# Kernel tuning notes

Hardware: AMD Instinct MI355X
Metric: run time of the kernel (lower is better)

## Reference

```python
import jax, jax.numpy as jnp
import numpy as np

N = 100_000      # nodes
E = 1_600_000    # edges
F_IN = 128       # n_features == conv_dim1..3
F_OUT = 256      # concat_dim
G = 2000         # number of graphs in the batch
EPS = 1e-5       # BatchNorm eps


def _xavier(k, shape):
    fan_in, fan_out = shape[-2], shape[-1]
    lim = float(np.sqrt(6.0 / (fan_in + fan_out)))
    return jax.random.uniform(k, shape, jnp.float32, -lim, lim)


def setup_inputs() -> dict:
    key = jax.random.key(0)
    ks = jax.random.split(key, 8)
    x = jax.random.normal(ks[0], (N, F_IN), jnp.float32)
    edge_index = jax.random.randint(ks[1], (2, E), 0, N, dtype=jnp.int64)
    batch = jnp.sort(jax.random.randint(ks[2], (N,), 0, G, dtype=jnp.int64))
    # layers 1..5: F_IN -> F_IN (stacked), layer 6: F_IN -> F_OUT
    Wi = _xavier(ks[3], (5, F_IN, F_IN))   # ARMA init_weight per layer
    Wr = _xavier(ks[4], (5, F_IN, F_IN))   # ARMA root_weight per layer
    b = jnp.zeros((5, F_IN), jnp.float32)  # ARMA bias per layer
    g = jnp.ones((5, F_IN), jnp.float32)   # BN gamma
    be = jnp.zeros((5, F_IN), jnp.float32) # BN beta
    Wi6 = _xavier(ks[5], (F_IN, F_OUT))
    Wr6 = _xavier(ks[6], (F_IN, F_OUT))
    b6 = jnp.zeros((F_OUT,), jnp.float32)
    g6 = jnp.ones((F_OUT,), jnp.float32)
    be6 = jnp.zeros((F_OUT,), jnp.float32)
    return dict(x=x, edge_index=edge_index, batch=batch, Wi=Wi, Wr=Wr, b=b,
                g=g, be=be, Wi6=Wi6, Wr6=Wr6, b6=b6, g6=g6, be6=be6)


def _arma(x, norm, row, col, Wi_l, Wr_l, b_l):
    # ARMAConv (num_stacks=1, num_layers=1, act=ReLU):
    #   out = ReLU( A_norm @ (x W_init) + x W_root + b )
    h = x @ Wi_l                                           # [N, F_out]
    msg = h[row] * norm[:, None]                           # gather + scale, [E, F_out]
    agg = jax.ops.segment_sum(msg, col, num_segments=N)    # scatter-add
    return jax.nn.relu(agg + x @ Wr_l + b_l)


def _bn(x, gamma, beta):
    # BatchNorm1d, training mode (biased batch variance)
    mu = x.mean(axis=0)
    var = x.var(axis=0)
    return gamma * (x - mu) * jax.lax.rsqrt(var + EPS) + beta


def reference(x, edge_index, batch, Wi, Wr, b, g, be, Wi6, Wr6, b6, g6, be6):
    row, col = edge_index[0], edge_index[1]
    # gcn_norm without self loops: D^-1/2 A D^-1/2 edge weights
    deg = jax.ops.segment_sum(jnp.ones((E,), x.dtype), col, num_segments=N)
    dinv = jnp.where(deg > 0, jax.lax.rsqrt(deg), 0.0)
    norm = dinv[row] * dinv[col]                           # [E]

    h = x
    for l in range(5):  # fixed small layer count
        h = _arma(h, norm, row, col, Wi[l], Wr[l], b[l])   # outer F.relu is idempotent
        h = _bn(h, g[l], be[l])
    h = _arma(h, norm, row, col, Wi6, Wr6, b6)
    h = _bn(h, g6, be6)
    # global_add_pool over graph ids; dropout = identity (deterministic baseline)
    out = jax.ops.segment_sum(h, batch, num_segments=G)    # [G, F_OUT]
    return out
```

## Files before the change

kernel.cpp:

```cpp
#include <hip/hip_runtime.h>

#define Nn 100000
#define NP 100001
#define Ee 1600000
#define Gg 2000
#define EPSf 1e-5f

typedef unsigned short ushort_t;
typedef __attribute__((ext_vector_type(8))) short short8;
typedef __attribute__((ext_vector_type(4))) float f32x4;
typedef __attribute__((ext_vector_type(4))) unsigned u32x4;

__device__ inline float bf2f(unsigned int u) {
    union { unsigned int i; float f; } v; v.i = u << 16; return v.f;
}
__device__ inline unsigned short f2bf(float f) {
    unsigned int x = __float_as_uint(f);
    unsigned int r = (x + 0x7fffu + ((x >> 16) & 1u)) >> 16;
    return (unsigned short)r;
}
__device__ inline int ldidx(const void* a, int i, int i64) {
    return i64 ? (int)((const long long*)a)[i] : ((const int*)a)[i];
}
__device__ inline float ldflt(const void* p, long long i, int f32) {
    return f32 ? ((const float*)p)[i] : bf2f(((const ushort_t*)p)[i]);
}


__global__ void k_flags(const void* gones, const void* ei, int* flags) {
    if (threadIdx.x == 0 && blockIdx.x == 0) {
        unsigned w = *(const unsigned*)gones;
        flags[0] = (w == 0x3F800000u) ? 1 : 0;
        const int* e = (const int*)ei;
        int nz = 0;
        for (int i = 0; i < 256; i++) nz |= e[2 * i + 1];
        flags[1] = nz ? 0 : 1;
    }
}


__global__ void k_hist(const void* __restrict__ ei, int* __restrict__ deg, const int* __restrict__ flags) {
    int i = blockIdx.x * 256 + threadIdx.x;
    if (i < Ee) {
        int c = ldidx(ei, Ee + i, flags[1]);
        atomicAdd(&deg[c], 1);
    }
}

__global__ void k_dinv(const int* __restrict__ deg, float* __restrict__ dinv) {
    int i = blockIdx.x * 256 + threadIdx.x;
    if (i < Nn) { int d = deg[i]; dinv[i] = d > 0 ? rsqrtf((float)d) : 0.f; }
}

__global__ void k_scan1(const int* __restrict__ deg, int* __restrict__ off, int* __restrict__ part) {
    __shared__ int sh[1024];
    int i = blockIdx.x * 1024 + threadIdx.x;
    int v = (i < Nn) ? ((deg[i] + 3) & ~3) : 0;
    sh[threadIdx.x] = v;
    __syncthreads();
    for (int ofs = 1; ofs < 1024; ofs <<= 1) {
        int t = 0;
        if ((int)threadIdx.x >= ofs) t = sh[threadIdx.x - ofs];
        __syncthreads();
        sh[threadIdx.x] += t;
        __syncthreads();
    }
    if (i < Nn) off[i] = sh[threadIdx.x] - v;
    if (threadIdx.x == 1023) part[blockIdx.x] = sh[1023];
}

__global__ void k_scan2(int* part, int nb) {
    if (threadIdx.x == 0 && blockIdx.x == 0) {
        int run = 0;
        for (int i = 0; i < nb; i++) { int t = part[i]; part[i] = run; run += t; }
        part[nb] = run;
    }
}

__global__ void k_scan3(int* __restrict__ off, const int* __restrict__ part, int* __restrict__ cursor) {
    int i = blockIdx.x * 256 + threadIdx.x;
    if (i < Nn) {
        int v = off[i] + part[i >> 10];
        off[i] = v;
        cursor[i] = v;
    }
    if (i == 0) off[Nn] = part[98];
}

__global__ void k_fillp(const void* __restrict__ ei, int* __restrict__ cursor,
                        int* __restrict__ srcS, const int* __restrict__ flags) {
    int range = blockIdx.x & 7;
    int e = (blockIdx.x >> 3) * 256 + threadIdx.x;
    if (e < Ee) {
        int i64 = flags[1];
        int c = ldidx(ei, Ee + e, i64);
        if (c >= range * 12500 && c < (range + 1) * 12500) {
            int r = ldidx(ei, e, i64);
            int p = atomicAdd(&cursor[c], 1);
            srcS[p] = r;
        }
    }
}

__global__ void k_pad(const int* __restrict__ cursor, const int* __restrict__ off,
                      int* __restrict__ srcS) {
    int i = blockIdx.x * 256 + threadIdx.x;
    if (i < Nn) {
        int e = off[i + 1];
        for (int p = cursor[i]; p < e; p++) srcS[p] = Nn;
    }
}

__global__ void k_zrow(ushort_t* __restrict__ Hi) {
    int t = threadIdx.x;
    int fc = t >> 4, j = t & 15;
    Hi[((size_t)fc * NP + Nn) * 16 + j] = 0;
}

__global__ void k_cvtp(const void* b, const void* b6, const void* g, const void* g6,
                       const void* be, const void* be6,
                       float* __restrict__ biasF, float* __restrict__ gF,
                       float* __restrict__ beF, const int* __restrict__ flags) {
    int i = blockIdx.x * 256 + threadIdx.x;
    if (i >= 2688) return;
    int grp = i / 896, r = i - grp * 896;
    int f32 = flags[0];
    const void* srcs[6] = { b, b6, g, g6, be, be6 };
    float* dsts[3] = { biasF, gF, beF };
    const void* s = (r < 640) ? srcs[grp * 2] : srcs[grp * 2 + 1];
    int idx = (r < 640) ? r : r - 640;
    dsts[grp][r] = ldflt(s, idx, f32);
}

__global__ void k_cvtx(const void* __restrict__ x, ushort_t* __restrict__ xq, const int* __restrict__ flags) {
    int node = blockIdx.x * 256 + threadIdx.x;
    int fc = blockIdx.y;
    if (node < Nn) {
        union { ushort_t u[16]; u32x4 v[2]; } t;
        if (flags[0]) {
            const float* p = (const float*)x + (size_t)node * 128 + fc * 16;
#pragma unroll
            for (int j = 0; j < 16; j++) t.u[j] = f2bf(p[j]);
        } else {
            const ushort_t* p = (const ushort_t*)x + (size_t)node * 128 + fc * 16;
#pragma unroll
            for (int j = 0; j < 16; j++) t.u[j] = p[j];
        }
        u32x4* d = (u32x4*)(xq + ((size_t)fc * Nn + node) * 16);
        d[0] = t.v[0]; d[1] = t.v[1];
    }
}

__global__ void k_pack(const void* __restrict__ Wi, const void* __restrict__ Wr,
                       const void* __restrict__ Wi6, const void* __restrict__ Wr6,
                       ushort_t* __restrict__ Bp, const int* __restrict__ flags) {
    int idx = blockIdx.x * 256 + threadIdx.x;
    if (idx >= 229376) return;
    int f32 = flags[0];
    if (idx < 163840) {
        int l = idx / 32768, rem = idx - l * 32768;
        int kg = rem / 2048, rem2 = rem - kg * 2048;
        int n = rem2 / 8, j = rem2 - n * 8;
        int k = kg * 8 + j;
        float v = (n < 128) ? ldflt(Wi, (l * 128 + k) * 128 + n, f32)
                            : ldflt(Wr, (l * 128 + k) * 128 + (n - 128), f32);
        Bp[idx] = f2bf(v);
    } else {
        int idx2 = idx - 163840;
        int kg = idx2 / 4096, rem2 = idx2 - kg * 4096;
        int n = rem2 / 8, j = rem2 - n * 8;
        int k = kg * 8 + j;
        float v = (n < 256) ? ldflt(Wi6, k * 256 + n, f32) : ldflt(Wr6, k * 256 + (n - 256), f32);
        Bp[idx] = f2bf(v);
    }
}

__global__ void k_fold(const ushort_t* __restrict__ Bp, const float* __restrict__ stat,
                       const float* __restrict__ gamma, const float* __restrict__ beta,
                       const float* __restrict__ bias,
                       ushort_t* __restrict__ Bp2, float* __restrict__ hcorr, int ncat) {
    __shared__ float red[128];
    int n = blockIdx.x, k = threadIdx.x;
    int fhalf = ncat >> 1;
    float mu = stat[k] * (1.f / Nn);
    float var = stat[128 + k] * (1.f / Nn) - mu * mu;
    float rs = rsqrtf(var + EPSf);
    float s = gamma[k] * rs;
    float h = beta[k] - s * mu;
    size_t idx = ((size_t)(k >> 3) * ncat + n) * 8 + (k & 7);
    float w = bf2f(Bp[idx]);
    Bp2[idx] = f2bf(w * s);
    red[k] = h * w;
    __syncthreads();
    for (int m = 64; m > 0; m >>= 1) { if (k < m) red[k] += red[k + m]; __syncthreads(); }
    if (k == 0) hcorr[n] = red[0] + (n >= fhalf ? bias[n - fhalf] : 0.f);
}

__global__ void k_h0(const float* __restrict__ bias, float* __restrict__ hc, int ncat) {
    int n = blockIdx.x * 256 + threadIdx.x;
    if (n < ncat) hc[n] = n >= (ncat >> 1) ? bias[n - (ncat >> 1)] : 0.f;
}


__global__ __launch_bounds__(256) void k_gemm(
        const ushort_t* __restrict__ Aq,
        const ushort_t* __restrict__ Bp, const float* __restrict__ hcorr,
        const float* __restrict__ dinv,
        ushort_t* __restrict__ Hi, ushort_t* __restrict__ yq, int ncat) {
    __shared__ ushort_t stage[32 * 264];
    const int tid = threadIdx.x, lane = tid & 63, wid = tid >> 6;
    const int q = lane >> 4, l15 = lane & 15;
    const int fhalf = ncat >> 1;
    const int colW = blockIdx.y * 256 + wid * 64;
    const int row0 = blockIdx.x * 64;

    short8 bfr[4][4];
    float hc[4];
#pragma unroll
    for (int kk = 0; kk < 4; kk++) {
        int kg = kk * 4 + q;
#pragma unroll
        for (int ct = 0; ct < 4; ct++)
            bfr[kk][ct] = *(const short8*)(Bp + ((size_t)kg * ncat + colW + ct * 16 + l15) * 8);
    }
#pragma unroll
    for (int ct = 0; ct < 4; ct++) hc[ct] = hcorr[colW + ct * 16 + l15];

    f32x4 acc[4][4];
    f32x4 z; z.x = 0.f; z.y = 0.f; z.z = 0.f; z.w = 0.f;
#pragma unroll
    for (int rt = 0; rt < 4; rt++)
#pragma unroll
        for (int ct = 0; ct < 4; ct++) acc[rt][ct] = z;

#pragma unroll
    for (int kk = 0; kk < 4; kk++) {
        int kg = kk * 4 + q;
        const ushort_t* ap = Aq + (size_t)(kg >> 1) * Nn * 16 + (kg & 1) * 8;
        short8 af[4];
#pragma unroll
        for (int rt = 0; rt < 4; rt++) {
            int node = row0 + rt * 16 + l15;
            if (node >= Nn) node = Nn - 1;
            af[rt] = *(const short8*)(ap + (size_t)node * 16);
        }
#pragma unroll
        for (int rt = 0; rt < 4; rt++)
#pragma unroll
            for (int ct = 0; ct < 4; ct++)
                acc[rt][ct] = __builtin_amdgcn_mfma_f32_16x16x32_bf16(af[rt], bfr[kk][ct], acc[rt][ct], 0, 0, 0);
    }

#pragma unroll
    for (int half = 0; half < 2; half++) {
        __syncthreads();
#pragma unroll
        for (int ct = 0; ct < 4; ct++) {
            int lcol = wid * 64 + ct * 16 + l15;
            bool isHi = (blockIdx.y * 256 + lcol) < fhalf;
#pragma unroll
            for (int rt2 = 0; rt2 < 2; rt2++) {
                int rt = half * 2 + rt2;
#pragma unroll
                for (int r = 0; r < 4; r++) {
                    int grow = row0 + rt * 16 + q * 4 + r;
                    int gr = grow < Nn ? grow : 0;
                    float v = acc[rt][ct][r] + hc[ct];
                    if (isHi) v *= dinv[gr];
                    stage[(rt2 * 16 + q * 4 + r) * 264 + lcol] = f2bf(v);
                }
            }
        }
        __syncthreads();
        for (int chunk = tid; chunk < 512; chunk += 256) {
            int cg = chunk & 15, rl = chunk >> 4;
            int node = row0 + half * 32 + rl;
            if (node < Nn) {
                int gc0 = blockIdx.y * 256 + cg * 16;
                const u32x4* sp = (const u32x4*)&stage[rl * 264 + cg * 16];
                u32x4 v0 = sp[0], v1 = sp[1];
                ushort_t* dst = (gc0 < fhalf)
                    ? Hi + ((size_t)(gc0 >> 4) * NP + node) * 16
                    : yq + ((size_t)((gc0 - fhalf) >> 4) * Nn + node) * 16;
                u32x4* dp = (u32x4*)dst;
                dp[0] = v0; dp[1] = v1;
            }
        }
    }
}


__global__ __launch_bounds__(256) void k_agg8(const int* __restrict__ off, const int* __restrict__ src,
                                              const float* __restrict__ dinv, const unsigned* __restrict__ Hi2,
                                              unsigned* __restrict__ yq, float* __restrict__ stat,
                                              int F, int fcbase) {
    const int tid = threadIdx.x;
    const int w = tid >> 6, lane = tid & 63;
    const int sub = lane >> 3, fl = lane & 7;
    const int e2 = (fl >> 1) & 3;
    const int h  = fl & 1;
    const int fc = fcbase + (blockIdx.x & 7);
    const int T = blockIdx.x >> 3;
    const char* __restrict__ gbase = (const char*)Hi2 + (size_t)fc * ((size_t)NP * 32) + h * 16;

    float stS[8], stQ[8];
#pragma unroll
    for (int j = 0; j < 8; j++) { stS[j] = 0.f; stQ[j] = 0.f; }

#pragma unroll
    for (int pass = 0; pass < 4; pass++) {
        int node = T * 128 + pass * 32 + w * 8 + sub;
        bool valid = node < Nn;
        int p0 = 0, p1 = 0;
        if (valid) { p0 = off[node]; p1 = off[node + 1]; }
        float a[8];
#pragma unroll
        for (int j = 0; j < 8; j++) a[j] = 0.f;
        int p = p0;
        for (; p + 15 < p1; p += 16) {
            int s0 = src[p + e2];
            int s1 = src[p + 4 + e2];
            int s2 = src[p + 8 + e2];
            int s3 = src[p + 12 + e2];
            u32x4 g0 = *(const u32x4*)(gbase + (size_t)((unsigned)s0 << 5));
            u32x4 g1 = *(const u32x4*)(gbase + (size_t)((unsigned)s1 << 5));
            u32x4 g2 = *(const u32x4*)(gbase + (size_t)((unsigned)s2 << 5));
            u32x4 g3 = *(const u32x4*)(gbase + (size_t)((unsigned)s3 << 5));
#pragma unroll
            for (int d = 0; d < 4; d++) {
                a[2*d]   += bf2f(g0[d] & 0xffffu); a[2*d+1] += bf2f(g0[d] >> 16);
                a[2*d]   += bf2f(g1[d] & 0xffffu); a[2*d+1] += bf2f(g1[d] >> 16);
                a[2*d]   += bf2f(g2[d] & 0xffffu); a[2*d+1] += bf2f(g2[d] >> 16);
                a[2*d]   += bf2f(g3[d] & 0xffffu); a[2*d+1] += bf2f(g3[d] >> 16);
            }
        }
        if (p + 7 < p1) {
            int s0 = src[p + e2];
            int s1 = src[p + 4 + e2];
            u32x4 g0 = *(const u32x4*)(gbase + (size_t)((unsigned)s0 << 5));
            u32x4 g1 = *(const u32x4*)(gbase + (size_t)((unsigned)s1 << 5));
#pragma unroll
            for (int d = 0; d < 4; d++) {
                a[2*d]   += bf2f(g0[d] & 0xffffu); a[2*d+1] += bf2f(g0[d] >> 16);
                a[2*d]   += bf2f(g1[d] & 0xffffu); a[2*d+1] += bf2f(g1[d] >> 16);
            }
            p += 8;
        }
        if (p < p1) {
            int s0 = src[p + e2];
            u32x4 g0 = *(const u32x4*)(gbase + (size_t)((unsigned)s0 << 5));
#pragma unroll
            for (int d = 0; d < 4; d++) {
                a[2*d]   += bf2f(g0[d] & 0xffffu); a[2*d+1] += bf2f(g0[d] >> 16);
            }
        }
#pragma unroll
        for (int j = 0; j < 8; j++) {
            a[j] += __shfl_xor(a[j], 2, 64);
            a[j] += __shfl_xor(a[j], 4, 64);
        }
        if (valid && fl < 2) {
            float dv = dinv[node];
            u32x4* yp = (u32x4*)(yq + ((size_t)fc * Nn + node) * 8 + h * 4);
            u32x4 uv = *yp;
#pragma unroll
            for (int d = 0; d < 4; d++) {
                float vlo = fmaxf(bf2f(uv[d] & 0xffffu) + dv * a[2*d],   0.f);
                float vhi = fmaxf(bf2f(uv[d] >> 16)     + dv * a[2*d+1], 0.f);
                uv[d] = (unsigned)f2bf(vlo) | ((unsigned)f2bf(vhi) << 16);
                stS[2*d]   += vlo; stQ[2*d]   += vlo * vlo;
                stS[2*d+1] += vhi; stQ[2*d+1] += vhi * vhi;
            }
            *yp = uv;
        }
    }
#pragma unroll
    for (int j = 0; j < 8; j++) {
        stS[j] += __shfl_xor(stS[j], 8, 64);
        stQ[j] += __shfl_xor(stQ[j], 8, 64);
        stS[j] += __shfl_xor(stS[j], 16, 64);
        stQ[j] += __shfl_xor(stQ[j], 16, 64);
        stS[j] += __shfl_xor(stS[j], 32, 64);
        stQ[j] += __shfl_xor(stQ[j], 32, 64);
    }
    __shared__ float red[4][2][8][2];
    if (lane < 2) {
#pragma unroll
        for (int j = 0; j < 8; j++) {
            red[w][lane][j][0] = stS[j];
            red[w][lane][j][1] = stQ[j];
        }
    }
    __syncthreads();
    if (tid < 32) {
        int hh = tid >> 4, r = tid & 15, j = r >> 1, m = r & 1;
        float s = red[0][hh][j][m] + red[1][hh][j][m] + red[2][hh][j][m] + red[3][hh][j][m];
        int f = fc * 16 + hh * 8 + j;
        atomicAdd(&stat[m * F + f], s);
    }
}


__device__ inline int lb(const void* a, int n, int key, int i64) {
    int lo = 0, hi = n;
    while (lo < hi) { int mid = (lo + hi) >> 1; if (ldidx(a, mid, i64) < key) lo = mid + 1; else hi = mid; }
    return lo;
}

__global__ void k_pool(const ushort_t* __restrict__ y6q, const float* __restrict__ stat,
                       const float* __restrict__ g6, const float* __restrict__ be6,
                       const void* __restrict__ batch, void* __restrict__ out,
                       const int* __restrict__ flags) {
    int g = blockIdx.x;
    int f = threadIdx.x;
    int i64 = flags[1];
    int start = lb(batch, Nn, g, i64);
    int end = lb(batch, Nn, g + 1, i64);
    const ushort_t* yp = y6q + (size_t)(f >> 4) * Nn * 16 + (f & 15);
    float s = 0.f;
    for (int n = start; n < end; n++) s += bf2f(yp[(size_t)n * 16]);
    int cnt = end - start;
    float mu = stat[f] * (1.f / Nn);
    float var = stat[256 + f] * (1.f / Nn) - mu * mu;
    float rs = rsqrtf(var + EPSf);
    float val = g6[f] * rs * (s - (float)cnt * mu) + (float)cnt * be6[f];
    if (flags[0]) ((float*)out)[(size_t)g * 256 + f] = val;
    else          ((ushort_t*)out)[(size_t)g * 256 + f] = f2bf(val);
}


extern "C" void kernel_launch(void* const* d_in, const int* in_sizes, int n_in,
                              void* d_out, int out_size, void* d_ws, size_t ws_size,
                              hipStream_t stream) {
    const void* x    = d_in[0];
    const void* ei   = d_in[1];
    const void* batch= d_in[2];
    const void* Wi   = d_in[3];
    const void* Wr   = d_in[4];
    const void* b    = d_in[5];
    const void* g    = d_in[6];
    const void* be   = d_in[7];
    const void* Wi6  = d_in[8];
    const void* Wr6  = d_in[9];
    const void* b6   = d_in[10];
    const void* g6   = d_in[11];
    const void* be6  = d_in[12];

    char* p = (char*)d_ws;
    auto alloc = [&](size_t bytes) { char* r = p; p += (bytes + 511) & ~(size_t)511; return r; };
    ushort_t* HiB  = (ushort_t*)alloc((size_t)NP * 256 * 2);
    ushort_t* xq   = (ushort_t*)alloc((size_t)Nn * 128 * 2);
    ushort_t* yAq  = (ushort_t*)alloc((size_t)Nn * 128 * 2);
    ushort_t* yBq  = (ushort_t*)alloc((size_t)Nn * 128 * 2);
    ushort_t* y6q  = (ushort_t*)alloc((size_t)Nn * 256 * 2);
    int* srcS      = (int*)alloc(((size_t)Ee + 4 * Nn + 64) * 4);
    int* off       = (int*)alloc((size_t)(Nn + 1) * 4);
    int* cursor    = (int*)alloc((size_t)Nn * 4);
    int* deg       = (int*)alloc((size_t)Nn * 4);
    float* dinv    = (float*)alloc((size_t)Nn * 4);
    int* part      = (int*)alloc(128 * 4);
    float* statsA  = (float*)alloc(6 * 512 * 4);
    ushort_t* Bp   = (ushort_t*)alloc(229376 * 2);
    ushort_t* Bp2  = (ushort_t*)alloc(65536 * 2);
    float* hcorrA  = (float*)alloc(512 * 4);
    int* flags     = (int*)alloc(2 * 4);
    float* biasF   = (float*)alloc(896 * 4);
    float* gF      = (float*)alloc(896 * 4);
    float* beF     = (float*)alloc(896 * 4);
    const unsigned* Hi2 = (const unsigned*)HiB;

    const int AGG_GRID = 782 * 8;
    const int GEMM_GRID = 1563;

    k_flags<<<1, 64, 0, stream>>>(g, ei, flags);
    k_cvtp<<<11, 256, 0, stream>>>(b, b6, g, g6, be, be6, biasF, gF, beF, flags);

    hipMemsetAsync(deg, 0, (size_t)Nn * 4, stream);
    hipMemsetAsync(statsA, 0, 6 * 512 * 4, stream);
    k_hist<<<6250, 256, 0, stream>>>(ei, deg, flags);
    k_dinv<<<391, 256, 0, stream>>>(deg, dinv);
    k_scan1<<<98, 1024, 0, stream>>>(deg, off, part);
    k_scan2<<<1, 64, 0, stream>>>(part, 98);
    k_scan3<<<391, 256, 0, stream>>>(off, part, cursor);
    k_fillp<<<50000, 256, 0, stream>>>(ei, cursor, srcS, flags);
    k_pad<<<391, 256, 0, stream>>>(cursor, off, srcS);
    k_zrow<<<1, 256, 0, stream>>>(HiB);
    k_pack<<<896, 256, 0, stream>>>(Wi, Wr, Wi6, Wr6, Bp, flags);
    k_cvtx<<<dim3(391, 8), 256, 0, stream>>>(x, xq, flags);
    k_h0<<<1, 256, 0, stream>>>(biasF, hcorrA, 256);

    k_gemm<<<dim3(GEMM_GRID, 1), 256, 0, stream>>>(xq, Bp, hcorrA, dinv, HiB, yAq, 256);
    k_agg8<<<AGG_GRID, 256, 0, stream>>>(off, srcS, dinv, Hi2, (unsigned*)yAq, statsA, 128, 0);
    k_fold<<<256, 128, 0, stream>>>(Bp + 32768, statsA, gF, beF, biasF + 128, Bp2, hcorrA, 256);

    k_gemm<<<dim3(GEMM_GRID, 1), 256, 0, stream>>>(yAq, Bp2, hcorrA, dinv, HiB, yBq, 256);
    k_agg8<<<AGG_GRID, 256, 0, stream>>>(off, srcS, dinv, Hi2, (unsigned*)yBq, statsA + 512, 128, 0);
    k_fold<<<256, 128, 0, stream>>>(Bp + 65536, statsA + 512, gF + 128, beF + 128, biasF + 256, Bp2, hcorrA, 256);

    k_gemm<<<dim3(GEMM_GRID, 1), 256, 0, stream>>>(yBq, Bp2, hcorrA, dinv, HiB, yAq, 256);
    k_agg8<<<AGG_GRID, 256, 0, stream>>>(off, srcS, dinv, Hi2, (unsigned*)yAq, statsA + 1024, 128, 0);
    k_fold<<<256, 128, 0, stream>>>(Bp + 98304, statsA + 1024, gF + 256, beF + 256, biasF + 384, Bp2, hcorrA, 256);

    k_gemm<<<dim3(GEMM_GRID, 1), 256, 0, stream>>>(yAq, Bp2, hcorrA, dinv, HiB, yBq, 256);
    k_agg8<<<AGG_GRID, 256, 0, stream>>>(off, srcS, dinv, Hi2, (unsigned*)yBq, statsA + 1536, 128, 0);
    k_fold<<<256, 128, 0, stream>>>(Bp + 131072, statsA + 1536, gF + 384, beF + 384, biasF + 512, Bp2, hcorrA, 256);

    k_gemm<<<dim3(GEMM_GRID, 1), 256, 0, stream>>>(yBq, Bp2, hcorrA, dinv, HiB, yAq, 256);
    k_agg8<<<AGG_GRID, 256, 0, stream>>>(off, srcS, dinv, Hi2, (unsigned*)yAq, statsA + 2048, 128, 0);
    k_fold<<<512, 128, 0, stream>>>(Bp + 163840, statsA + 2048, gF + 512, beF + 512, biasF + 640, Bp2, hcorrA, 512);

    k_gemm<<<dim3(GEMM_GRID, 2), 256, 0, stream>>>(yAq, Bp2, hcorrA, dinv, HiB, y6q, 512);
    k_agg8<<<AGG_GRID, 256, 0, stream>>>(off, srcS, dinv, Hi2, (unsigned*)y6q, statsA + 2560, 256, 0);
    k_agg8<<<AGG_GRID, 256, 0, stream>>>(off, srcS, dinv, Hi2, (unsigned*)y6q, statsA + 2560, 256, 8);
    k_pool<<<Gg, 256, 0, stream>>>(y6q, statsA + 2560, gF + 640, be6 ? beF + 640 : beF + 640, batch, d_out, flags);
}
```

Before: 1.145 ms.

## Split CSR aggregation by source-node half and widen feature planes to 32

Edges are partitioned into two CSRs by source index (below or above 50000), and aggregation runs in two passes. The first pass writes fp32 partial sums into scratch buffers, and the second adds the other half and applies the ReLU epilogue and BN statistics. Each pass gathers from only half the node rows, which is meant to keep the gathered working set resident in cache. Feature planes are also widened from 16 to 32 bf16 (64-byte rows) across the GEMM, conversion and pooling code. In exchange it adds extra launches, a second scan/fill pipeline, and fp32 partial-sum write and read traffic, and it reuses activation buffers as scratch.

```diff
diff --git a/kernel.cpp b/kernel.cpp
--- a/kernel.cpp
+++ b/kernel.cpp
@@ -5,6 +5,7 @@
 #define Ee 1600000
 #define Gg 2000
 #define EPSf 1e-5f
+#define NHALF 50000
 
 typedef unsigned short ushort_t;
 typedef __attribute__((ext_vector_type(8))) short short8;
@@ -39,17 +40,21 @@
 }
 
 
-__global__ void k_hist(const void* __restrict__ ei, int* __restrict__ deg, const int* __restrict__ flags) {
+__global__ void k_hist(const void* __restrict__ ei, int* __restrict__ degA, int* __restrict__ degB,
+                       const int* __restrict__ flags) {
     int i = blockIdx.x * 256 + threadIdx.x;
     if (i < Ee) {
-        int c = ldidx(ei, Ee + i, flags[1]);
-        atomicAdd(&deg[c], 1);
-    }
-}
-
-__global__ void k_dinv(const int* __restrict__ deg, float* __restrict__ dinv) {
+        int i64 = flags[1];
+        int c = ldidx(ei, Ee + i, i64);
+        int r = ldidx(ei, i, i64);
+        atomicAdd((r < NHALF) ? &degA[c] : &degB[c], 1);
+    }
+}
+
+__global__ void k_dinv(const int* __restrict__ degA, const int* __restrict__ degB,
+                       float* __restrict__ dinv) {
     int i = blockIdx.x * 256 + threadIdx.x;
-    if (i < Nn) { int d = deg[i]; dinv[i] = d > 0 ? rsqrtf((float)d) : 0.f; }
+    if (i < Nn) { int d = degA[i] + degB[i]; dinv[i] = d > 0 ? rsqrtf((float)d) : 0.f; }
 }
 
 __global__ void k_scan1(const int* __restrict__ deg, int* __restrict__ off, int* __restrict__ part) {
@@ -87,8 +92,8 @@
     if (i == 0) off[Nn] = part[98];
 }
 
-__global__ void k_fillp(const void* __restrict__ ei, int* __restrict__ cursor,
-                        int* __restrict__ srcS, const int* __restrict__ flags) {
+__global__ void k_fillp(const void* __restrict__ ei, int* __restrict__ curA, int* __restrict__ curB,
+                        int* __restrict__ srcA, int* __restrict__ srcB, const int* __restrict__ flags) {
     int range = blockIdx.x & 7;
     int e = (blockIdx.x >> 3) * 256 + threadIdx.x;
     if (e < Ee) {
@@ -96,25 +101,29 @@
         int c = ldidx(ei, Ee + e, i64);
         if (c >= range * 12500 && c < (range + 1) * 12500) {
             int r = ldidx(ei, e, i64);
-            int p = atomicAdd(&cursor[c], 1);
-            srcS[p] = r;
-        }
-    }
-}
-
-__global__ void k_pad(const int* __restrict__ cursor, const int* __restrict__ off,
-                      int* __restrict__ srcS) {
+            if (r < NHALF) { int p = atomicAdd(&curA[c], 1); srcA[p] = r; }
+            else           { int p = atomicAdd(&curB[c], 1); srcB[p] = r; }
+        }
+    }
+}
+
+__global__ void k_pad(const int* __restrict__ curA, const int* __restrict__ offA, int* __restrict__ srcA,
+                      const int* __restrict__ curB, const int* __restrict__ offB, int* __restrict__ srcB) {
     int i = blockIdx.x * 256 + threadIdx.x;
     if (i < Nn) {
-        int e = off[i + 1];
-        for (int p = cursor[i]; p < e; p++) srcS[p] = Nn;
-    }
-}
-
-__global__ void k_zrow(ushort_t* __restrict__ Hi) {
+        int e = offA[i + 1];
+        for (int p = curA[i]; p < e; p++) srcA[p] = Nn;
+        e = offB[i + 1];
+        for (int p = curB[i]; p < e; p++) srcB[p] = Nn;
+    }
+}
+
+__global__ void k_zrow(unsigned* __restrict__ Hi) {
     int t = threadIdx.x;
-    int fc = t >> 4, j = t & 15;
-    Hi[((size_t)fc * NP + Nn) * 16 + j] = 0;
+    if (t < 128) {
+        int pl = t >> 4, j = t & 15;
+        Hi[((size_t)pl * NP + Nn) * 16 + j] = 0;
+    }
 }
 
 __global__ void k_cvtp(const void* b, const void* b6, const void* g, const void* g6,
@@ -146,7 +155,7 @@
 #pragma unroll
             for (int j = 0; j < 16; j++) t.u[j] = p[j];
         }
-        u32x4* d = (u32x4*)(xq + ((size_t)fc * Nn + node) * 16);
+        u32x4* d = (u32x4*)(xq + ((size_t)(fc >> 1) * Nn + node) * 32 + (fc & 1) * 16);
         d[0] = t.v[0]; d[1] = t.v[1];
     }
 }
@@ -236,13 +245,13 @@
 #pragma unroll
     for (int kk = 0; kk < 4; kk++) {
         int kg = kk * 4 + q;
-        const ushort_t* ap = Aq + (size_t)(kg >> 1) * Nn * 16 + (kg & 1) * 8;
+        const ushort_t* ap = Aq + (size_t)(kg >> 2) * ((size_t)Nn * 32) + (kg & 3) * 8;
         short8 af[4];
 #pragma unroll
         for (int rt = 0; rt < 4; rt++) {
             int node = row0 + rt * 16 + l15;
             if (node >= Nn) node = Nn - 1;
-            af[rt] = *(const short8*)(ap + (size_t)node * 16);
+            af[rt] = *(const short8*)(ap + (size_t)node * 32);
         }
 #pragma unroll
         for (int rt = 0; rt < 4; rt++)
@@ -279,9 +288,13 @@
                 int gc0 = blockIdx.y * 256 + cg * 16;
                 const u32x4* sp = (const u32x4*)&stage[rl * 264 + cg * 16];
                 u32x4 v0 = sp[0], v1 = sp[1];
-                ushort_t* dst = (gc0 < fhalf)
-                    ? Hi + ((size_t)(gc0 >> 4) * NP + node) * 16
-                    : yq + ((size_t)((gc0 - fhalf) >> 4) * Nn + node) * 16;
+                ushort_t* dst;
+                if (gc0 < fhalf) {
+                    dst = Hi + ((size_t)(gc0 >> 5) * NP + node) * 32 + (gc0 & 16);
+                } else {
+                    int gy = gc0 - fhalf;
+                    dst = yq + ((size_t)(gy >> 5) * Nn + node) * 32 + (gy & 16);
+                }
                 u32x4* dp = (u32x4*)dst;
                 dp[0] = v0; dp[1] = v1;
             }
@@ -290,22 +303,79 @@
 }
 
 
-__global__ __launch_bounds__(256) void k_agg8(const int* __restrict__ off, const int* __restrict__ src,
-                                              const float* __restrict__ dinv, const unsigned* __restrict__ Hi2,
-                                              unsigned* __restrict__ yq, float* __restrict__ stat,
-                                              int F, int fcbase) {
+__device__ __forceinline__ void edge_sum(const int* __restrict__ src, int p0, int p1,
+                                         const char* __restrict__ gbase, int e2,
+                                         float* __restrict__ a) {
+    int p = p0;
+    for (; p + 15 < p1; p += 16) {
+        int b0 = p + 2 * e2;
+        int sa0 = src[b0],      sa1 = src[b0 + 1];
+        int sb0 = src[b0 + 4],  sb1 = src[b0 + 5];
+        int sc0 = src[b0 + 8],  sc1 = src[b0 + 9];
+        int sd0 = src[b0 + 12], sd1 = src[b0 + 13];
+        u32x4 g0 = *(const u32x4*)(gbase + ((size_t)(unsigned)sa0 << 6));
+        u32x4 g1 = *(const u32x4*)(gbase + ((size_t)(unsigned)sa1 << 6));
+        u32x4 g2 = *(const u32x4*)(gbase + ((size_t)(unsigned)sb0 << 6));
+        u32x4 g3 = *(const u32x4*)(gbase + ((size_t)(unsigned)sb1 << 6));
+        u32x4 g4 = *(const u32x4*)(gbase + ((size_t)(unsigned)sc0 << 6));
+        u32x4 g5 = *(const u32x4*)(gbase + ((size_t)(unsigned)sc1 << 6));
+        u32x4 g6 = *(const u32x4*)(gbase + ((size_t)(unsigned)sd0 << 6));
+        u32x4 g7 = *(const u32x4*)(gbase + ((size_t)(unsigned)sd1 << 6));
+#pragma unroll
+        for (int d = 0; d < 4; d++) {
+            a[2*d] += bf2f(g0[d] & 0xffffu); a[2*d+1] += bf2f(g0[d] >> 16);
+            a[2*d] += bf2f(g1[d] & 0xffffu); a[2*d+1] += bf2f(g1[d] >> 16);
+            a[2*d] += bf2f(g2[d] & 0xffffu); a[2*d+1] += bf2f(g2[d] >> 16);
+            a[2*d] += bf2f(g3[d] & 0xffffu); a[2*d+1] += bf2f(g3[d] >> 16);
+            a[2*d] += bf2f(g4[d] & 0xffffu); a[2*d+1] += bf2f(g4[d] >> 16);
+            a[2*d] += bf2f(g5[d] & 0xffffu); a[2*d+1] += bf2f(g5[d] >> 16);
+            a[2*d] += bf2f(g6[d] & 0xffffu); a[2*d+1] += bf2f(g6[d] >> 16);
+            a[2*d] += bf2f(g7[d] & 0xffffu); a[2*d+1] += bf2f(g7[d] >> 16);
+        }
+    }
+    if (p + 7 < p1) {
+        int b0 = p + 2 * e2;
+        int sa0 = src[b0],     sa1 = src[b0 + 1];
+        int sb0 = src[b0 + 4], sb1 = src[b0 + 5];
+        u32x4 g0 = *(const u32x4*)(gbase + ((size_t)(unsigned)sa0 << 6));
+        u32x4 g1 = *(const u32x4*)(gbase + ((size_t)(unsigned)sa1 << 6));
+        u32x4 g2 = *(const u32x4*)(gbase + ((size_t)(unsigned)sb0 << 6));
+        u32x4 g3 = *(const u32x4*)(gbase + ((size_t)(unsigned)sb1 << 6));
+#pragma unroll
+        for (int d = 0; d < 4; d++) {
+            a[2*d] += bf2f(g0[d] & 0xffffu); a[2*d+1] += bf2f(g0[d] >> 16);
+            a[2*d] += bf2f(g1[d] & 0xffffu); a[2*d+1] += bf2f(g1[d] >> 16);
+            a[2*d] += bf2f(g2[d] & 0xffffu); a[2*d+1] += bf2f(g2[d] >> 16);
+            a[2*d] += bf2f(g3[d] & 0xffffu); a[2*d+1] += bf2f(g3[d] >> 16);
+        }
+        p += 8;
+    }
+    if (p < p1) {
+        int b0 = p + 2 * e2;
+        int sa0 = src[b0], sa1 = src[b0 + 1];
+        u32x4 g0 = *(const u32x4*)(gbase + ((size_t)(unsigned)sa0 << 6));
+        u32x4 g1 = *(const u32x4*)(gbase + ((size_t)(unsigned)sa1 << 6));
+#pragma unroll
+        for (int d = 0; d < 4; d++) {
+            a[2*d] += bf2f(g0[d] & 0xffffu); a[2*d+1] += bf2f(g0[d] >> 16);
+            a[2*d] += bf2f(g1[d] & 0xffffu); a[2*d+1] += bf2f(g1[d] >> 16);
+        }
+    }
+}
+
+__global__ __launch_bounds__(256) void k_aggA(const int* __restrict__ off, const int* __restrict__ src,
+                                              const unsigned* __restrict__ Hi2,
+                                              float* __restrict__ pAlo, float* __restrict__ pAhi,
+                                              int fcpbase) {
     const int tid = threadIdx.x;
     const int w = tid >> 6, lane = tid & 63;
     const int sub = lane >> 3, fl = lane & 7;
-    const int e2 = (fl >> 1) & 3;
-    const int h  = fl & 1;
-    const int fc = fcbase + (blockIdx.x & 7);
-    const int T = blockIdx.x >> 3;
-    const char* __restrict__ gbase = (const char*)Hi2 + (size_t)fc * ((size_t)NP * 32) + h * 16;
-
-    float stS[8], stQ[8];
-#pragma unroll
-    for (int j = 0; j < 8; j++) { stS[j] = 0.f; stQ[j] = 0.f; }
+    const int e2 = fl >> 2, qd = fl & 3;
+    const int combo = blockIdx.x & 7;
+    const int fcl = combo & 3;
+    const int T = (blockIdx.x >> 3) + 391 * (combo >> 2);
+    const char* __restrict__ gbase = (const char*)Hi2 + (size_t)(fcpbase + fcl) * ((size_t)NP * 64) + qd * 16;
+    float* __restrict__ pbase = ((fcl & 2) ? pAhi : pAlo) + (size_t)(fcl & 1) * ((size_t)Nn * 32) + qd * 8;
 
 #pragma unroll
     for (int pass = 0; pass < 4; pass++) {
@@ -316,62 +386,69 @@
         float a[8];
 #pragma unroll
         for (int j = 0; j < 8; j++) a[j] = 0.f;
-        int p = p0;
-        for (; p + 15 < p1; p += 16) {
-            int s0 = src[p + e2];
-            int s1 = src[p + 4 + e2];
-            int s2 = src[p + 8 + e2];
-            int s3 = src[p + 12 + e2];
-            u32x4 g0 = *(const u32x4*)(gbase + (size_t)((unsigned)s0 << 5));
-            u32x4 g1 = *(const u32x4*)(gbase + (size_t)((unsigned)s1 << 5));
-            u32x4 g2 = *(const u32x4*)(gbase + (size_t)((unsigned)s2 << 5));
-            u32x4 g3 = *(const u32x4*)(gbase + (size_t)((unsigned)s3 << 5));
+        edge_sum(src, p0, p1, gbase, e2, a);
+#pragma unroll
+        for (int j = 0; j < 8; j++) a[j] += __shfl_xor(a[j], 4, 64);
+        if (valid && e2 == 0) {
+            float* pr = pbase + (size_t)node * 32;
+            f32x4 v0, v1;
+            v0.x = a[0]; v0.y = a[1]; v0.z = a[2]; v0.w = a[3];
+            v1.x = a[4]; v1.y = a[5]; v1.z = a[6]; v1.w = a[7];
+            *(f32x4*)pr = v0;
+            *(f32x4*)(pr + 4) = v1;
+        }
+    }
+}
+
+__global__ __launch_bounds__(256) void k_aggB(const int* __restrict__ off, const int* __restrict__ src,
+                                              const float* __restrict__ dinv, const unsigned* __restrict__ Hi2,
+                                              const float* __restrict__ pAlo, const float* __restrict__ pAhi,
+                                              unsigned* __restrict__ yq, float* __restrict__ stat,
+                                              int F, int fcpbase) {
+    const int tid = threadIdx.x;
+    const int w = tid >> 6, lane = tid & 63;
+    const int sub = lane >> 3, fl = lane & 7;
+    const int e2 = fl >> 2, qd = fl & 3;
+    const int combo = blockIdx.x & 7;
+    const int fcl = combo & 3;
+    const int fcp = fcpbase + fcl;
+    const int T = (blockIdx.x >> 3) + 391 * (combo >> 2);
+    const char* __restrict__ gbase = (const char*)Hi2 + (size_t)fcp * ((size_t)NP * 64) + qd * 16;
+    const float* __restrict__ pbase = ((fcl & 2) ? pAhi : pAlo) + (size_t)(fcl & 1) * ((size_t)Nn * 32) + qd * 8;
+
+    float stS[8], stQ[8];
+#pragma unroll
+    for (int j = 0; j < 8; j++) { stS[j] = 0.f; stQ[j] = 0.f; }
+
+#pragma unroll
+    for (int pass = 0; pass < 4; pass++) {
+        int node = T * 128 + pass * 32 + w * 8 + sub;
+        bool valid = node < Nn;
+        int p0 = 0, p1 = 0;
+        if (valid) { p0 = off[node]; p1 = off[node + 1]; }
+        float a[8];
+#pragma unroll
+        for (int j = 0; j < 8; j++) a[j] = 0.f;
+        edge_sum(src, p0, p1, gbase, e2, a);
+#pragma unroll
+        for (int j = 0; j < 8; j++) a[j] += __shfl_xor(a[j], 4, 64);
+        if (valid && e2 == 0) {
+            float dv = dinv[node];
+            const float* pr = pbase + (size_t)node * 32;
+            f32x4 pa0 = *(const f32x4*)pr;
+            f32x4 pa1 = *(const f32x4*)(pr + 4);
+            float pav[8] = { pa0.x, pa0.y, pa0.z, pa0.w, pa1.x, pa1.y, pa1.z, pa1.w };
+            unsigned* yp = yq + ((size_t)fcp * Nn + node) * 16 + qd * 4;
+            u32x4 uv = *(u32x4*)yp;
 #pragma unroll
             for (int d = 0; d < 4; d++) {
-                a[2*d]   += bf2f(g0[d] & 0xffffu); a[2*d+1] += bf2f(g0[d] >> 16);
-                a[2*d]   += bf2f(g1[d] & 0xffffu); a[2*d+1] += bf2f(g1[d] >> 16);
-                a[2*d]   += bf2f(g2[d] & 0xffffu); a[2*d+1] += bf2f(g2[d] >> 16);
-                a[2*d]   += bf2f(g3[d] & 0xffffu); a[2*d+1] += bf2f(g3[d] >> 16);
-            }
-        }
-        if (p + 7 < p1) {
-            int s0 = src[p + e2];
-            int s1 = src[p + 4 + e2];
-            u32x4 g0 = *(const u32x4*)(gbase + (size_t)((unsigned)s0 << 5));
-            u32x4 g1 = *(const u32x4*)(gbase + (size_t)((unsigned)s1 << 5));
-#pragma unroll
-            for (int d = 0; d < 4; d++) {
-                a[2*d]   += bf2f(g0[d] & 0xffffu); a[2*d+1] += bf2f(g0[d] >> 16);
-                a[2*d]   += bf2f(g1[d] & 0xffffu); a[2*d+1] += bf2f(g1[d] >> 16);
-            }
-            p += 8;
-        }
-        if (p < p1) {
-            int s0 = src[p + e2];
-            u32x4 g0 = *(const u32x4*)(gbase + (size_t)((unsigned)s0 << 5));
-#pragma unroll
-            for (int d = 0; d < 4; d++) {
-                a[2*d]   += bf2f(g0[d] & 0xffffu); a[2*d+1] += bf2f(g0[d] >> 16);
-            }
-        }
-#pragma unroll
-        for (int j = 0; j < 8; j++) {
-            a[j] += __shfl_xor(a[j], 2, 64);
-            a[j] += __shfl_xor(a[j], 4, 64);
-        }
-        if (valid && fl < 2) {
-            float dv = dinv[node];
-            u32x4* yp = (u32x4*)(yq + ((size_t)fc * Nn + node) * 8 + h * 4);
-            u32x4 uv = *yp;
-#pragma unroll
-            for (int d = 0; d < 4; d++) {
-                float vlo = fmaxf(bf2f(uv[d] & 0xffffu) + dv * a[2*d],   0.f);
-                float vhi = fmaxf(bf2f(uv[d] >> 16)     + dv * a[2*d+1], 0.f);
+                float vlo = fmaxf(bf2f(uv[d] & 0xffffu) + dv * (pav[2*d]   + a[2*d]),   0.f);
+                float vhi = fmaxf(bf2f(uv[d] >> 16)     + dv * (pav[2*d+1] + a[2*d+1]), 0.f);
                 uv[d] = (unsigned)f2bf(vlo) | ((unsigned)f2bf(vhi) << 16);
                 stS[2*d]   += vlo; stQ[2*d]   += vlo * vlo;
                 stS[2*d+1] += vhi; stQ[2*d+1] += vhi * vhi;
             }
-            *yp = uv;
+            *(u32x4*)yp = uv;
         }
     }
 #pragma unroll
@@ -383,8 +460,8 @@
         stS[j] += __shfl_xor(stS[j], 32, 64);
         stQ[j] += __shfl_xor(stQ[j], 32, 64);
     }
-    __shared__ float red[4][2][8][2];
-    if (lane < 2) {
+    __shared__ float red[4][4][8][2];
+    if (lane < 4) {
 #pragma unroll
         for (int j = 0; j < 8; j++) {
             red[w][lane][j][0] = stS[j];
@@ -392,11 +469,10 @@
         }
     }
     __syncthreads();
-    if (tid < 32) {
-        int hh = tid >> 4, r = tid & 15, j = r >> 1, m = r & 1;
-        float s = red[0][hh][j][m] + red[1][hh][j][m] + red[2][hh][j][m] + red[3][hh][j][m];
-        int f = fc * 16 + hh * 8 + j;
-        atomicAdd(&stat[m * F + f], s);
+    if (tid < 64) {
+        int qdx = tid >> 4, j = (tid >> 1) & 7, m = tid & 1;
+        float s = red[0][qdx][j][m] + red[1][qdx][j][m] + red[2][qdx][j][m] + red[3][qdx][j][m];
+        atomicAdd(&stat[m * F + fcp * 32 + qdx * 8 + j], s);
     }
 }
 
@@ -416,9 +492,9 @@
     int i64 = flags[1];
     int start = lb(batch, Nn, g, i64);
     int end = lb(batch, Nn, g + 1, i64);
-    const ushort_t* yp = y6q + (size_t)(f >> 4) * Nn * 16 + (f & 15);
+    const ushort_t* yp = y6q + (size_t)(f >> 5) * ((size_t)Nn * 32) + (f & 31);
     float s = 0.f;
-    for (int n = start; n < end; n++) s += bf2f(yp[(size_t)n * 16]);
+    for (int n = start; n < end; n++) s += bf2f(yp[(size_t)n * 32]);
     int cnt = end - start;
     float mu = stat[f] * (1.f / Nn);
     float var = stat[256 + f] * (1.f / Nn) - mu * mu;
@@ -453,12 +529,17 @@
     ushort_t* yAq  = (ushort_t*)alloc((size_t)Nn * 128 * 2);
     ushort_t* yBq  = (ushort_t*)alloc((size_t)Nn * 128 * 2);
     ushort_t* y6q  = (ushort_t*)alloc((size_t)Nn * 256 * 2);
-    int* srcS      = (int*)alloc(((size_t)Ee + 4 * Nn + 64) * 4);
-    int* off       = (int*)alloc((size_t)(Nn + 1) * 4);
-    int* cursor    = (int*)alloc((size_t)Nn * 4);
-    int* deg       = (int*)alloc((size_t)Nn * 4);
+    int* srcA      = (int*)alloc(((size_t)Ee + 4 * Nn + 64) * 4);
+    int* srcB      = (int*)alloc(((size_t)Ee + 4 * Nn + 64) * 4);
+    int* offA      = (int*)alloc((size_t)(Nn + 1) * 4);
+    int* offB      = (int*)alloc((size_t)(Nn + 1) * 4);
+    int* curA      = (int*)alloc((size_t)Nn * 4);
+    int* curB      = (int*)alloc((size_t)Nn * 4);
+    int* degA      = (int*)alloc((size_t)Nn * 4);
+    int* degB      = (int*)alloc((size_t)Nn * 4);
     float* dinv    = (float*)alloc((size_t)Nn * 4);
-    int* part      = (int*)alloc(128 * 4);
+    int* partA     = (int*)alloc(128 * 4);
+    int* partB     = (int*)alloc(128 * 4);
     float* statsA  = (float*)alloc(6 * 512 * 4);
     ushort_t* Bp   = (ushort_t*)alloc(229376 * 2);
     ushort_t* Bp2  = (ushort_t*)alloc(65536 * 2);
@@ -469,48 +550,64 @@
     float* beF     = (float*)alloc(896 * 4);
     const unsigned* Hi2 = (const unsigned*)HiB;
 
-    const int AGG_GRID = 782 * 8;
+    float* pAlo = (float*)y6q;
+    float* pAhi = (float*)((char*)y6q + (size_t)Nn * 256);
+    float* p5lo = (float*)xq;
+    float* p5hi = (float*)yBq;
+
+    const int AGG_GRID = 8 * 391;
     const int GEMM_GRID = 1563;
 
     k_flags<<<1, 64, 0, stream>>>(g, ei, flags);
     k_cvtp<<<11, 256, 0, stream>>>(b, b6, g, g6, be, be6, biasF, gF, beF, flags);
 
-    hipMemsetAsync(deg, 0, (size_t)Nn * 4, stream);
+    hipMemsetAsync(degA, 0, (size_t)Nn * 4, stream);
+    hipMemsetAsync(degB, 0, (size_t)Nn * 4, stream);
     hipMemsetAsync(statsA, 0, 6 * 512 * 4, stream);
-    k_hist<<<6250, 256, 0, stream>>>(ei, deg, flags);
-    k_dinv<<<391, 256, 0, stream>>>(deg, dinv);
-    k_scan1<<<98, 1024, 0, stream>>>(deg, off, part);
-    k_scan2<<<1, 64, 0, stream>>>(part, 98);
-    k_scan3<<<391, 256, 0, stream>>>(off, part, cursor);
-    k_fillp<<<50000, 256, 0, stream>>>(ei, cursor, srcS, flags);
-    k_pad<<<391, 256, 0, stream>>>(cursor, off, srcS);
-    k_zrow<<<1, 256, 0, stream>>>(HiB);
+    k_hist<<<6250, 256, 0, stream>>>(ei, degA, degB, flags);
+    k_dinv<<<391, 256, 0, stream>>>(degA, degB, dinv);
+    k_scan1<<<98, 1024, 0, stream>>>(degA, offA, partA);
+    k_scan2<<<1, 64, 0, stream>>>(partA, 98);
+    k_scan3<<<391, 256, 0, stream>>>(offA, partA, curA);
+    k_scan1<<<98, 1024, 0, stream>>>(degB, offB, partB);
+    k_scan2<<<1, 64, 0, stream>>>(partB, 98);
+    k_scan3<<<391, 256, 0, stream>>>(offB, partB, curB);
+    k_fillp<<<50000, 256, 0, stream>>>(ei, curA, curB, srcA, srcB, flags);
+    k_pad<<<391, 256, 0, stream>>>(curA, offA, srcA, curB, offB, srcB);
+    k_zrow<<<1, 256, 0, stream>>>((unsigned*)HiB);
     k_pack<<<896, 256, 0, stream>>>(Wi, Wr, Wi6, Wr6, Bp, flags);
     k_cvtx<<<dim3(391, 8), 256, 0, stream>>>(x, xq, flags);
     k_h0<<<1, 256, 0, stream>>>(biasF, hcorrA, 256);
 
     k_gemm<<<dim3(GEMM_GRID, 1), 256, 0, stream>>>(xq, Bp, hcorrA, dinv, HiB, yAq, 256);
-    k_agg8<<<AGG_GRID, 256, 0, stream>>>(off, srcS, dinv, Hi2, (unsigned*)yAq, statsA, 128, 0);
+    k_aggA<<<AGG_GRID, 256, 0, stream>>>(offA, srcA, Hi2, pAlo, pAhi, 0);
+    k_aggB<<<AGG_GRID, 256, 0, stream>>>(offB, srcB, dinv, Hi2, pAlo, pAhi, (unsigned*)yAq, statsA, 128, 0);
     k_fold<<<256, 128, 0, stream>>>(Bp + 32768, statsA, gF, beF, biasF + 128, Bp2, hcorrA, 256);
 
     k_gemm<<<dim3(GEMM_GRID, 1), 256, 0, stream>>>(yAq, Bp2, hcorrA, dinv, HiB, yBq, 256);
-    k_agg8<<<AGG_GRID, 256, 0, stream>>>(off, srcS, dinv, Hi2, (unsigned*)yBq, statsA + 512, 128, 0);
+    k_aggA<<<AGG_GRID, 256, 0, stream>>>(offA, srcA, Hi2, pAlo, pAhi, 0);
+    k_aggB<<<AGG_GRID, 256, 0, stream>>>(offB, srcB, dinv, Hi2, pAlo, pAhi, (unsigned*)yBq, statsA + 512, 128, 0);
     k_fold<<<256, 128, 0, stream>>>(Bp + 65536, statsA + 512, gF + 128, beF + 128, biasF + 256, Bp2, hcorrA, 256);
 
     k_gemm<<<dim3(GEMM_GRID, 1), 256, 0, stream>>>(yBq, Bp2, hcorrA, dinv, HiB, yAq, 256);
-    k_agg8<<<AGG_GRID, 256, 0, stream>>>(off, srcS, dinv, Hi2, (unsigned*)yAq, statsA + 1024, 128, 0);
+    k_aggA<<<AGG_GRID, 256, 0, stream>>>(offA, srcA, Hi2, pAlo, pAhi, 0);
+    k_aggB<<<AGG_GRID, 256, 0, stream>>>(offB, srcB, dinv, Hi2, pAlo, pAhi, (unsigned*)yAq, statsA + 1024, 128, 0);
     k_fold<<<256, 128, 0, stream>>>(Bp + 98304, statsA + 1024, gF + 256, beF + 256, biasF + 384, Bp2, hcorrA, 256);
 
     k_gemm<<<dim3(GEMM_GRID, 1), 256, 0, stream>>>(yAq, Bp2, hcorrA, dinv, HiB, yBq, 256);
-    k_agg8<<<AGG_GRID, 256, 0, stream>>>(off, srcS, dinv, Hi2, (unsigned*)yBq, statsA + 1536, 128, 0);
+    k_aggA<<<AGG_GRID, 256, 0, stream>>>(offA, srcA, Hi2, pAlo, pAhi, 0);
+    k_aggB<<<AGG_GRID, 256, 0, stream>>>(offB, srcB, dinv, Hi2, pAlo, pAhi, (unsigned*)yBq, statsA + 1536, 128, 0);
     k_fold<<<256, 128, 0, stream>>>(Bp + 131072, statsA + 1536, gF + 384, beF + 384, biasF + 512, Bp2, hcorrA, 256);
 
     k_gemm<<<dim3(GEMM_GRID, 1), 256, 0, stream>>>(yBq, Bp2, hcorrA, dinv, HiB, yAq, 256);
-    k_agg8<<<AGG_GRID, 256, 0, stream>>>(off, srcS, dinv, Hi2, (unsigned*)yAq, statsA + 2048, 128, 0);
+    k_aggA<<<AGG_GRID, 256, 0, stream>>>(offA, srcA, Hi2, pAlo, pAhi, 0);
+    k_aggB<<<AGG_GRID, 256, 0, stream>>>(offB, srcB, dinv, Hi2, pAlo, pAhi, (unsigned*)yAq, statsA + 2048, 128, 0);
     k_fold<<<512, 128, 0, stream>>>(Bp + 163840, statsA + 2048, gF + 512, beF + 512, biasF + 640, Bp2, hcorrA, 512);
 
     k_gemm<<<dim3(GEMM_GRID, 2), 256, 0, stream>>>(yAq, Bp2, hcorrA, dinv, HiB, y6q, 512);
-    k_agg8<<<AGG_GRID, 256, 0, stream>>>(off, srcS, dinv, Hi2, (unsigned*)y6q, statsA + 2560, 256, 0);
-    k_agg8<<<AGG_GRID, 256, 0, stream>>>(off, srcS, dinv, Hi2, (unsigned*)y6q, statsA + 2560, 256, 8);
-    k_pool<<<Gg, 256, 0, stream>>>(y6q, statsA + 2560, gF + 640, be6 ? beF + 640 : beF + 640, batch, d_out, flags);
-}
+    k_aggA<<<AGG_GRID, 256, 0, stream>>>(offA, srcA, Hi2, p5lo, p5hi, 0);
+    k_aggB<<<AGG_GRID, 256, 0, stream>>>(offB, srcB, dinv, Hi2, p5lo, p5hi, (unsigned*)y6q, statsA + 2560, 256, 0);
+    k_aggA<<<AGG_GRID, 256, 0, stream>>>(offA, srcA, Hi2, p5lo, p5hi, 4);
+    k_aggB<<<AGG_GRID, 256, 0, stream>>>(offB, srcB, dinv, Hi2, p5lo, p5hi, (unsigned*)y6q, statsA + 2560, 256, 4);
+    k_pool<<<Gg, 256, 0, stream>>>(y6q, statsA + 2560, gF + 640, beF + 640, batch, d_out, flags);
+}
```

Result: slower. 1.247 ms (+9.0%).
